# Kernel tuning notes

Hardware: AMD Instinct MI355X
Metric: run time of the kernel (lower is better)

The kernel has to match this reference:

```python
import jax, jax.numpy as jnp
import numpy as np

NUM_EXPERTS = 8
TOP_K = 2
RMS_EPS = 1e-6
SCALING = NUM_EXPERTS / TOP_K


def setup_inputs() -> dict:
    key = jax.random.key(0)
    ks = jax.random.split(key, 6)
    B, S, H, I, E = 4, 2048, 2048, 1024, NUM_EXPERTS
    return {
        "hidden_states": jax.random.normal(ks[0], (B, S, H), dtype=jnp.float32),
        "norm_w": jnp.ones((H,), dtype=jnp.float32),
        "router_w": jax.random.normal(ks[1], (E, H), dtype=jnp.float32) * 0.02,
        "gate_w": jax.random.normal(ks[2], (E, I, H), dtype=jnp.float32) * 0.02,
        "up_w": jax.random.normal(ks[3], (E, I, H), dtype=jnp.float32) * 0.02,
        "down_w": jax.random.normal(ks[4], (E, H, I), dtype=jnp.float32) * 0.02,
    }


def reference(hidden_states, norm_w, router_w, gate_w, up_w, down_w):
    B, S, H = hidden_states.shape
    T = B * S
    flat = hidden_states.reshape(T, H)

    # RMSNorm on router input (fp32 math, as in torch module)
    x32 = flat.astype(jnp.float32)
    var = jnp.mean(x32 * x32, axis=-1, keepdims=True)
    router_input = norm_w * (x32 * jax.lax.rsqrt(var + RMS_EPS))

    # Router: softmax -> top-k -> renormalize
    logits = router_input @ router_w.T                     # [T, E]
    probs = jax.nn.softmax(logits, axis=-1)
    topw, topi = jax.lax.top_k(probs, TOP_K)               # [T, K]
    topw = topw / jnp.sum(topw, axis=-1, keepdims=True)

    # Expert combine: per-token weight for expert e (0 if not selected).
    # Running every token through every expert with weight-0 masking is
    # mathematically identical to the gather/scatter dispatch.
    out = jnp.zeros_like(flat)
    for e in range(NUM_EXPERTS):
        w_e = jnp.sum(jnp.where(topi == e, topw, 0.0), axis=-1)   # [T]
        g = flat @ gate_w[e].T                                    # [T, I]
        u = flat @ up_w[e].T                                      # [T, I]
        o = (jax.nn.silu(g) * u) @ down_w[e].T                    # [T, H]
        out = out + o * w_e[:, None]

    student_output = out.reshape(B, S, H) * SCALING

    # Aux load-balancing loss (training path)
    importance = jnp.sum(probs, axis=0) / T                       # [E]
    load = jnp.sum(topi[..., None] == jnp.arange(NUM_EXPERTS), axis=(0, 1)) / (T * TOP_K)
    aux_loss = jnp.sum(importance * load.astype(jnp.float32)) * NUM_EXPERTS

    return student_output, aux_loss
```

## Files before the change

### kernel.cpp

```cpp
#include <hip/hip_runtime.h>
#include <hip/hip_bf16.h>
#include <cstdint>

#define T_TOKENS 8192
#define H_DIM 2048
#define I_DIM 1024
#define N_EXPERTS 8
#define PAIRS (T_TOKENS * 2)
#define TOT_TILES 144
#define TOT_ROWS (TOT_TILES * 128)

using f32x4 = __attribute__((ext_vector_type(4))) float;
using bfv   = __attribute__((ext_vector_type(8))) short;
using u16x8 = __attribute__((ext_vector_type(8))) unsigned short;

typedef __attribute__((address_space(3))) unsigned int lds_u32;
typedef __attribute__((address_space(1))) unsigned int glb_u32;

__device__ __forceinline__ void gll16(const void* g, void* l) {
  __builtin_amdgcn_global_load_lds((const glb_u32*)g, (lds_u32*)l, 16, 0, 0);
}
#define SB0() __builtin_amdgcn_sched_barrier(0)
#define BAR() __builtin_amdgcn_s_barrier()

__device__ inline unsigned short f2bf(float f) {
  unsigned int u = __float_as_uint(f);
  u += 0x7FFFu + ((u >> 16) & 1u);
  return (unsigned short)(u >> 16);
}
__device__ inline float bf2f(unsigned short u) {
  return __uint_as_float((unsigned int)u << 16);
}

__global__ __launch_bounds__(256) void moe_convert_kernel(
    const float* __restrict__ src, unsigned short* __restrict__ dst, int n8) {
  int i = blockIdx.x * 256 + threadIdx.x;
  if (i >= n8) return;
  size_t o = (size_t)i * 8;
  f32x4 a = *reinterpret_cast<const f32x4*>(src + o);
  f32x4 b = *reinterpret_cast<const f32x4*>(src + o + 4);
  u16x8 r = {f2bf(a[0]), f2bf(a[1]), f2bf(a[2]), f2bf(a[3]),
             f2bf(b[0]), f2bf(b[1]), f2bf(b[2]), f2bf(b[3])};
  *reinterpret_cast<u16x8*>(dst + o) = r;
}

__global__ __launch_bounds__(256) void moe_router_kernel(
    const float* __restrict__ X, const float* __restrict__ norm_w,
    const float* __restrict__ rw, float* __restrict__ probs,
    float* __restrict__ topw, int* __restrict__ topi,
    unsigned int* __restrict__ counts, unsigned short* __restrict__ Xb,
    const float* __restrict__ gate_w, const float* __restrict__ up_w,
    const float* __restrict__ down_w,
    unsigned short* __restrict__ W1, unsigned short* __restrict__ W2,
    unsigned short* __restrict__ W3) {
  int t = blockIdx.x;
  int tid = threadIdx.x;
  {
    size_t co = (size_t)t * 2048 + tid * 8;
    f32x4 a = *reinterpret_cast<const f32x4*>(gate_w + co);
    f32x4 b = *reinterpret_cast<const f32x4*>(gate_w + co + 4);
    u16x8 r = {f2bf(a[0]), f2bf(a[1]), f2bf(a[2]), f2bf(a[3]),
               f2bf(b[0]), f2bf(b[1]), f2bf(b[2]), f2bf(b[3])};
    *reinterpret_cast<u16x8*>(W1 + co) = r;
    a = *reinterpret_cast<const f32x4*>(up_w + co);
    b = *reinterpret_cast<const f32x4*>(up_w + co + 4);
    u16x8 r2 = {f2bf(a[0]), f2bf(a[1]), f2bf(a[2]), f2bf(a[3]),
                f2bf(b[0]), f2bf(b[1]), f2bf(b[2]), f2bf(b[3])};
    *reinterpret_cast<u16x8*>(W2 + co) = r2;
    if (W3) {
      a = *reinterpret_cast<const f32x4*>(down_w + co);
      b = *reinterpret_cast<const f32x4*>(down_w + co + 4);
      u16x8 r3 = {f2bf(a[0]), f2bf(a[1]), f2bf(a[2]), f2bf(a[3]),
                  f2bf(b[0]), f2bf(b[1]), f2bf(b[2]), f2bf(b[3])};
      *reinterpret_cast<u16x8*>(W3 + co) = r3;
    }
  }
  const float* x = X + (size_t)t * H_DIM;
  int base = tid * 8;
  f32x4 v0 = *reinterpret_cast<const f32x4*>(x + base);
  f32x4 v1 = *reinterpret_cast<const f32x4*>(x + base + 4);
  u16x8 bx = {f2bf(v0[0]), f2bf(v0[1]), f2bf(v0[2]), f2bf(v0[3]),
              f2bf(v1[0]), f2bf(v1[1]), f2bf(v1[2]), f2bf(v1[3])};
  *reinterpret_cast<u16x8*>(Xb + (size_t)t * H_DIM + base) = bx;
  f32x4 nw0 = *reinterpret_cast<const f32x4*>(norm_w + base);
  f32x4 nw1 = *reinterpret_cast<const f32x4*>(norm_w + base + 4);
  float vals[9];
  vals[0] = v0[0]*v0[0] + v0[1]*v0[1] + v0[2]*v0[2] + v0[3]*v0[3]
          + v1[0]*v1[0] + v1[1]*v1[1] + v1[2]*v1[2] + v1[3]*v1[3];
  f32x4 a0 = v0 * nw0, a1 = v1 * nw1;
#pragma unroll
  for (int e = 0; e < 8; ++e) {
    const float* r = rw + e * H_DIM + base;
    f32x4 r0 = *reinterpret_cast<const f32x4*>(r);
    f32x4 r1 = *reinterpret_cast<const f32x4*>(r + 4);
    f32x4 d = a0 * r0 + a1 * r1;
    vals[e + 1] = d[0] + d[1] + d[2] + d[3];
  }
#pragma unroll
  for (int v = 0; v < 9; ++v) {
    float s = vals[v];
#pragma unroll
    for (int off = 32; off > 0; off >>= 1) s += __shfl_xor(s, off);
    vals[v] = s;
  }
  __shared__ float red[4][9];
  int lane = tid & 63, w = tid >> 6;
  if (lane == 0) {
#pragma unroll
    for (int v = 0; v < 9; ++v) red[w][v] = vals[v];
  }
  __syncthreads();
  if (tid == 0) {
    float tot[9];
#pragma unroll
    for (int v = 0; v < 9; ++v) tot[v] = red[0][v] + red[1][v] + red[2][v] + red[3][v];
    float rs = rsqrtf(tot[0] / (float)H_DIM + 1e-6f);
    float lg[8], mx = -1e30f;
#pragma unroll
    for (int e = 0; e < 8; ++e) { lg[e] = tot[e + 1] * rs; mx = fmaxf(mx, lg[e]); }
    float pe[8], sum = 0.f;
#pragma unroll
    for (int e = 0; e < 8; ++e) { pe[e] = expf(lg[e] - mx); sum += pe[e]; }
    float inv = 1.f / sum;
#pragma unroll
    for (int e = 0; e < 8; ++e) { pe[e] *= inv; probs[t * 8 + e] = pe[e]; }
    int b1 = 0; float p1 = pe[0];
#pragma unroll
    for (int e = 1; e < 8; ++e) if (pe[e] > p1) { p1 = pe[e]; b1 = e; }
    int b2 = -1; float p2 = -1.f;
#pragma unroll
    for (int e = 0; e < 8; ++e) if (e != b1 && pe[e] > p2) { p2 = pe[e]; b2 = e; }
    float wsum = p1 + p2;
    topw[t * 2] = p1 / wsum;
    topw[t * 2 + 1] = p2 / wsum;
    topi[t * 2] = b1;
    topi[t * 2 + 1] = b2;
    atomicAdd(&counts[b1], 1u);
    atomicAdd(&counts[8 + b2], 1u);
  }
}

__global__ __launch_bounds__(256) void moe_importance_kernel(
    const float* __restrict__ probs, float* __restrict__ impSum) {
  int e = blockIdx.x, tid = threadIdx.x;
  float s = 0.f;
  for (int t = tid; t < T_TOKENS; t += 256) s += probs[t * 8 + e];
  __shared__ float red[256];
  red[tid] = s;
  __syncthreads();
  for (int st = 128; st > 0; st >>= 1) {
    if (tid < st) red[tid] += red[tid + st];
    __syncthreads();
  }
  if (tid == 0) impSum[e] = red[0];
}

__global__ void moe_offsets_aux_kernel(const unsigned int* __restrict__ counts,
                                       const float* __restrict__ impSum,
                                       int* __restrict__ tileOff,
                                       float* __restrict__ out_aux) {
  if (threadIdx.x == 0 && blockIdx.x == 0) {
    int acc = 0;
    for (int b = 0; b < 16; ++b) {
      tileOff[b] = acc;
      acc += (int)((counts[b] + 127u) >> 7);
    }
    tileOff[16] = acc;
    float a = 0.f;
    for (int e = 0; e < 8; ++e) {
      float load = (float)(counts[e] + counts[8 + e]) / (float)PAIRS;
      a += (impSum[e] / (float)T_TOKENS) * load;
    }
    out_aux[0] = a * (float)N_EXPERTS;
  }
}

__global__ __launch_bounds__(256) void moe_assign_kernel(
    const int* __restrict__ topi, const int* __restrict__ tileOff,
    unsigned int* __restrict__ cursors, int* __restrict__ row2pair) {
  int p = blockIdx.x * 256 + threadIdx.x;
  if (p >= PAIRS) return;
  int b = topi[p] + 8 * (p & 1);
  unsigned int pos = atomicAdd(&cursors[b], 1u);
  row2pair[tileOff[b] * 128 + (int)pos] = p;
}


__global__ __launch_bounds__(256, 4) void moe_stage_a(
    const unsigned short* __restrict__ Xb,
    const unsigned short* __restrict__ Wg, const unsigned short* __restrict__ Wu,
    const int* __restrict__ row2pair, const int* __restrict__ tileOff,
    unsigned int* __restrict__ workCtr, unsigned short* __restrict__ P) {
  __shared__ __align__(16) unsigned short sAB[16384];
  __shared__ int sTok[128];
  __shared__ int sWork;
  const int tid = threadIdx.x;
  const int lane = tid & 63, w = tid >> 6;
  const int wm = w >> 1, wn = w & 1;
  const int lrow = lane & 15, grp = lane >> 4;
  const int sub = lane >> 3;
  const int kcs = ((lane & 7) ^ sub) << 3;
  const int cx = (lane & 7) << 3;
  const int nTiles = tileOff[16];
  const int nWork = nTiles * 16;

  for (;;) {
    if (tid == 0) sWork = (int)atomicAdd(workCtr, 1u);
    __syncthreads();
    const int item = sWork;
    if (item >= nWork) break;
    const int mt = item >> 4;
    const int nt = item & 15;
    int b = 0;
#pragma unroll
    for (int k = 1; k < 16; ++k) if (tileOff[k] <= mt) b = k;
    const int e = b & 7;
    const int row0 = mt * 128;
    if (tid < 128) {
      int pr = row2pair[row0 + tid];
      sTok[tid] = (pr >= 0) ? (pr >> 1) : 0;
    }
    __syncthreads();

    const size_t wbase = (size_t)e * ((size_t)I_DIM * H_DIM);
    const unsigned short* src[8];
#pragma unroll
    for (int i = 0; i < 4; ++i) {
      int row = i * 32 + 8 * w + sub;
      src[i] = Xb + (size_t)sTok[row] * H_DIM + kcs;
    }
#pragma unroll
    for (int i = 4; i < 8; ++i) {
      int brow = (i - 4) * 32 + 8 * w + sub;
      int wq = brow >> 6, r6 = brow & 63;
      int ic = nt * 64 + wq * 32 + (r6 & 31);
      const unsigned short* bp = (r6 & 32) ? Wu : Wg;
      src[i] = bp + wbase + (size_t)ic * H_DIM + kcs;
    }

    f32x4 acc[4][4] = {};

#pragma unroll 1
    for (int kk = 0; kk < 32; ++kk) {
#pragma unroll
      for (int i = 0; i < 8; ++i)
        gll16(src[i] + (kk << 6), (void*)&sAB[(i * 256 + tid) * 8]);
      SB0();
      asm volatile("s_waitcnt vmcnt(0)" ::: "memory");
      SB0();
      BAR();
      SB0();
#pragma unroll
      for (int ks = 0; ks < 2; ++ks) {
        const int co = ((ks * 4 + grp) << 3) ^ cx;
        bfv af[4], bf[4];
#pragma unroll
        for (int m = 0; m < 4; ++m)
          af[m] = *reinterpret_cast<const bfv*>(
              &sAB[(wm * 64 + m * 16 + lrow) * 64 + co]);
#pragma unroll
        for (int n = 0; n < 4; ++n)
          bf[n] = *reinterpret_cast<const bfv*>(
              &sAB[8192 + (wn * 64 + n * 16 + lrow) * 64 + co]);
        __builtin_amdgcn_s_setprio(1);
#pragma unroll
        for (int m = 0; m < 4; ++m)
#pragma unroll
          for (int n = 0; n < 4; ++n)
            acc[m][n] = __builtin_amdgcn_mfma_f32_16x16x32_bf16(af[m], bf[n], acc[m][n], 0, 0, 0);
        __builtin_amdgcn_s_setprio(0);
      }
      SB0();
      BAR();
    }

#pragma unroll
    for (int m = 0; m < 4; ++m) {
#pragma unroll
      for (int n = 0; n < 2; ++n) {
#pragma unroll
        for (int j = 0; j < 4; ++j) {
          float g = acc[m][n][j];
          float uu = acc[m][n + 2][j];
          float pv = (g / (1.f + expf(-g))) * uu;
          int row = row0 + wm * 64 + m * 16 + grp * 4 + j;
          int col = nt * 64 + wn * 32 + n * 16 + lrow;
          P[(size_t)row * I_DIM + col] = f2bf(pv);
        }
      }
    }
  }
}

__global__ __launch_bounds__(256, 4) void moe_stage_b(
    const unsigned short* __restrict__ Pb, const unsigned short* __restrict__ Wd,
    const int* __restrict__ row2pair, const int* __restrict__ tileOff,
    unsigned int* __restrict__ workCtr, unsigned short* __restrict__ Opairs) {
  __shared__ __align__(16) unsigned short sAB[16384];
  __shared__ int sPair[128];
  __shared__ int sWork;
  const int tid = threadIdx.x;
  const int lane = tid & 63, w = tid >> 6;
  const int wm = w >> 1, wn = w & 1;
  const int lrow = lane & 15, grp = lane >> 4;
  const int sub = lane >> 3;
  const int kcs = ((lane & 7) ^ sub) << 3;
  const int cx = (lane & 7) << 3;
  const int nTiles = tileOff[16];
  const int nWork = nTiles * 16;

  for (;;) {
    if (tid == 0) sWork = (int)atomicAdd(workCtr, 1u);
    __syncthreads();
    const int item = sWork;
    if (item >= nWork) break;
    const int mt = item >> 4;
    const int nt = item & 15;
    int b = 0;
#pragma unroll
    for (int k = 1; k < 16; ++k) if (tileOff[k] <= mt) b = k;
    const int e = b & 7;
    const int row0 = mt * 128, h0 = nt * 128;
    if (tid < 128) sPair[tid] = row2pair[row0 + tid];
    __syncthreads();

    const unsigned short* src[8];
#pragma unroll
    for (int i = 0; i < 4; ++i) {
      int row = i * 32 + 8 * w + sub;
      src[i] = Pb + (size_t)(row0 + row) * I_DIM + kcs;
    }
#pragma unroll
    for (int i = 4; i < 8; ++i) {
      int brow = (i - 4) * 32 + 8 * w + sub;
      src[i] = Wd + (size_t)e * ((size_t)H_DIM * I_DIM) + (size_t)(h0 + brow) * I_DIM + kcs;
    }

    f32x4 acc[4][4] = {};

#pragma unroll 1
    for (int kk = 0; kk < 16; ++kk) {
#pragma unroll
      for (int i = 0; i < 8; ++i)
        gll16(src[i] + (kk << 6), (void*)&sAB[(i * 256 + tid) * 8]);
      SB0();
      asm volatile("s_waitcnt vmcnt(0)" ::: "memory");
      SB0();
      BAR();
      SB0();
#pragma unroll
      for (int ks = 0; ks < 2; ++ks) {
        const int co = ((ks * 4 + grp) << 3) ^ cx;
        bfv af[4], bf[4];
#pragma unroll
        for (int m = 0; m < 4; ++m)
          af[m] = *reinterpret_cast<const bfv*>(
              &sAB[(wm * 64 + m * 16 + lrow) * 64 + co]);
#pragma unroll
        for (int n = 0; n < 4; ++n)
          bf[n] = *reinterpret_cast<const bfv*>(
              &sAB[8192 + (wn * 64 + n * 16 + lrow) * 64 + co]);
        __builtin_amdgcn_s_setprio(1);
#pragma unroll
        for (int m = 0; m < 4; ++m)
#pragma unroll
          for (int n = 0; n < 4; ++n)
            acc[m][n] = __builtin_amdgcn_mfma_f32_16x16x32_bf16(af[m], bf[n], acc[m][n], 0, 0, 0);
        __builtin_amdgcn_s_setprio(0);
      }
      SB0();
      BAR();
    }

#pragma unroll
    for (int m = 0; m < 4; ++m) {
#pragma unroll
      for (int j = 0; j < 4; ++j) {
        int rl = wm * 64 + m * 16 + grp * 4 + j;
        int pr = sPair[rl];
        if (pr < 0) continue;
        unsigned short* orow = Opairs + (size_t)pr * H_DIM + h0 + wn * 64 + lrow;
#pragma unroll
        for (int n = 0; n < 4; ++n) orow[n * 16] = f2bf(acc[m][n][j]);
      }
    }
  }
}

__global__ __launch_bounds__(256) void moe_combine_kernel(
    const unsigned short* __restrict__ Opairs, const float* __restrict__ topw,
    float* __restrict__ out) {
  size_t g = (size_t)blockIdx.x * 256 + threadIdx.x;
  size_t base = g * 8;
  int t = (int)(base >> 11);
  int h = (int)(base & 2047);
  float w0 = topw[t * 2] * 4.f;
  float w1 = topw[t * 2 + 1] * 4.f;
  u16x8 o0 = *reinterpret_cast<const u16x8*>(Opairs + (size_t)(t * 2) * H_DIM + h);
  u16x8 o1 = *reinterpret_cast<const u16x8*>(Opairs + (size_t)(t * 2 + 1) * H_DIM + h);
  f32x4 r0, r1;
#pragma unroll
  for (int j = 0; j < 4; ++j) r0[j] = w0 * bf2f(o0[j]) + w1 * bf2f(o1[j]);
#pragma unroll
  for (int j = 0; j < 4; ++j) r1[j] = w0 * bf2f(o0[4 + j]) + w1 * bf2f(o1[4 + j]);
  *reinterpret_cast<f32x4*>(out + base) = r0;
  *reinterpret_cast<f32x4*>(out + base + 4) = r1;
}

extern "C" void kernel_launch(void* const* d_in, const int* in_sizes, int n_in,
                              void* d_out, int out_size, void* d_ws, size_t ws_size,
                              hipStream_t stream) {
  const float* X = (const float*)d_in[0];
  const float* norm_w = (const float*)d_in[1];
  const float* router_w = (const float*)d_in[2];
  const float* gate_w = (const float*)d_in[3];
  const float* up_w = (const float*)d_in[4];
  const float* down_w = (const float*)d_in[5];
  float* out = (float*)d_out;

  char* ws = (char*)d_ws;
  unsigned short* P = (unsigned short*)(ws);
  float* probs = (float*)(ws + 37748736);
  float* topw = (float*)(ws + 38010880);
  int* topi = (int*)(ws + 38076416);
  int* row2pair = (int*)(ws + 38141952);
  char* ctrl = ws + 38215680;
  unsigned int* counts = (unsigned int*)(ctrl);
  unsigned int* cursors = (unsigned int*)(ctrl + 64);
  float* impSum = (float*)(ctrl + 128);
  int* tileOff = (int*)(ctrl + 192);
  unsigned int* wcA = (unsigned int*)(ctrl + 384);
  unsigned int* wcB = (unsigned int*)(ctrl + 388);
  unsigned short* W1 = (unsigned short*)(ws + 38216192);
  unsigned short* W2 = (unsigned short*)(ws + 71770624);
  unsigned short* Xb = (unsigned short*)(ws + 105325056);
  unsigned short* Opairs = (unsigned short*)(ws + 71770624);
  unsigned short* W3 = (unsigned short*)(ws + 138879488);
  const bool w3ok = ws_size >= 172433920ull;

  hipMemsetAsync(ctrl, 0, 512, stream);
  hipMemsetAsync(row2pair, 0xFF, (size_t)TOT_ROWS * 4, stream);

  moe_router_kernel<<<T_TOKENS, 256, 0, stream>>>(
      X, norm_w, router_w, probs, topw, topi, counts, Xb,
      gate_w, up_w, down_w, W1, W2, w3ok ? W3 : nullptr);
  moe_importance_kernel<<<N_EXPERTS, 256, 0, stream>>>(probs, impSum);
  moe_offsets_aux_kernel<<<1, 64, 0, stream>>>(counts, impSum, tileOff, out + 16777216);
  moe_assign_kernel<<<PAIRS / 256, 256, 0, stream>>>(topi, tileOff, cursors, row2pair);

  moe_stage_a<<<1024, 256, 0, stream>>>(Xb, W1, W2, row2pair, tileOff, wcA, P);

  const unsigned short* DW = W3;
  if (!w3ok) {
    const int N8 = (N_EXPERTS * I_DIM * H_DIM) / 8;
    moe_convert_kernel<<<N8 / 256, 256, 0, stream>>>(down_w, W1, N8);
    DW = W1;
  }
  moe_stage_b<<<1024, 256, 0, stream>>>(P, DW, row2pair, tileOff, wcB, Opairs);
  moe_combine_kernel<<<T_TOKENS, 256, 0, stream>>>(Opairs, topw, out);
}
```

Baseline: 623.2 us.

## Use 512-thread 128x256 tiles with 3-stage LDS prefetch pipeline in expert GEMMs

Both expert GEMM stages now run 512-thread workgroups that each compute a 128x256 output tile, doubling the N extent per work item and halving the number of items. Global-to-LDS loads are triple-buffered: three K-slices are issued up front and each iteration waits only for the oldest one (partial vmcnt) before prefetching the slice three steps ahead. This targets the exposed memory latency of the old load-then-wait-all loop and cuts redundant A-tile reloads. In exchange it uses much more LDS per block with one block per CU, and fewer, larger work items may balance less evenly across CUs.

```diff
diff --git a/kernel.cpp b/kernel.cpp
--- a/kernel.cpp
+++ b/kernel.cpp
@@ -9,6 +9,7 @@
 #define PAIRS (T_TOKENS * 2)
 #define TOT_TILES 144
 #define TOT_ROWS (TOT_TILES * 128)
+#define SLOT 24576
 
 using f32x4 = __attribute__((ext_vector_type(4))) float;
 using bfv   = __attribute__((ext_vector_type(8))) short;
@@ -186,31 +187,30 @@
 }
 
 
-__global__ __launch_bounds__(256, 4) void moe_stage_a(
+__global__ __launch_bounds__(512, 1) void moe_stage_a(
     const unsigned short* __restrict__ Xb,
     const unsigned short* __restrict__ Wg, const unsigned short* __restrict__ Wu,
     const int* __restrict__ row2pair, const int* __restrict__ tileOff,
     unsigned int* __restrict__ workCtr, unsigned short* __restrict__ P) {
-  __shared__ __align__(16) unsigned short sAB[16384];
+  __shared__ __align__(16) unsigned short sAB[3 * SLOT];
   __shared__ int sTok[128];
   __shared__ int sWork;
   const int tid = threadIdx.x;
   const int lane = tid & 63, w = tid >> 6;
-  const int wm = w >> 1, wn = w & 1;
+  const int wm = w >> 2, wn = w & 3;
   const int lrow = lane & 15, grp = lane >> 4;
-  const int sub = lane >> 3;
-  const int kcs = ((lane & 7) ^ sub) << 3;
+  const int r8 = tid >> 3, j8 = tid & 7;
   const int cx = (lane & 7) << 3;
   const int nTiles = tileOff[16];
-  const int nWork = nTiles * 16;
+  const int nWork = nTiles * 8;
 
   for (;;) {
     if (tid == 0) sWork = (int)atomicAdd(workCtr, 1u);
     __syncthreads();
     const int item = sWork;
     if (item >= nWork) break;
-    const int mt = item >> 4;
-    const int nt = item & 15;
+    const int mt = item >> 3;
+    const int nt = item & 7;
     int b = 0;
 #pragma unroll
     for (int k = 1; k < 16; ++k) if (tileOff[k] <= mt) b = k;
@@ -223,30 +223,41 @@
     __syncthreads();
 
     const size_t wbase = (size_t)e * ((size_t)I_DIM * H_DIM);
-    const unsigned short* src[8];
-#pragma unroll
-    for (int i = 0; i < 4; ++i) {
-      int row = i * 32 + 8 * w + sub;
-      src[i] = Xb + (size_t)sTok[row] * H_DIM + kcs;
-    }
-#pragma unroll
-    for (int i = 4; i < 8; ++i) {
-      int brow = (i - 4) * 32 + 8 * w + sub;
-      int wq = brow >> 6, r6 = brow & 63;
-      int ic = nt * 64 + wq * 32 + (r6 & 31);
-      const unsigned short* bp = (r6 & 32) ? Wu : Wg;
-      src[i] = bp + wbase + (size_t)ic * H_DIM + kcs;
+    const unsigned short* sA[2];
+    const unsigned short* sB[4];
+#pragma unroll
+    for (int i = 0; i < 2; ++i) {
+      int row = i * 64 + r8;
+      sA[i] = Xb + (size_t)sTok[row] * H_DIM + ((j8 ^ (row & 7)) << 3);
+    }
+    {
+      const unsigned short* bp = (r8 & 32) ? Wu : Wg;
+#pragma unroll
+      for (int i = 0; i < 4; ++i) {
+        int ic = nt * 128 + i * 32 + (r8 & 31);
+        sB[i] = bp + wbase + (size_t)ic * H_DIM + ((j8 ^ (r8 & 7)) << 3);
+      }
     }
 
     f32x4 acc[4][4] = {};
 
+#pragma unroll
+    for (int t = 0; t < 3; ++t) {
+      const int so = t * SLOT;
+#pragma unroll
+      for (int i = 0; i < 2; ++i)
+        gll16(sA[i] + (t << 6), (void*)&sAB[so + (i * 512 + tid) * 8]);
+#pragma unroll
+      for (int i = 0; i < 4; ++i)
+        gll16(sB[i] + (t << 6), (void*)&sAB[so + 8192 + (i * 512 + tid) * 8]);
+    }
+
+    int so = 0;
 #pragma unroll 1
     for (int kk = 0; kk < 32; ++kk) {
-#pragma unroll
-      for (int i = 0; i < 8; ++i)
-        gll16(src[i] + (kk << 6), (void*)&sAB[(i * 256 + tid) * 8]);
-      SB0();
-      asm volatile("s_waitcnt vmcnt(0)" ::: "memory");
+      if (kk < 30)      { asm volatile("s_waitcnt vmcnt(12)" ::: "memory"); }
+      else if (kk == 30){ asm volatile("s_waitcnt vmcnt(6)" ::: "memory"); }
+      else              { asm volatile("s_waitcnt vmcnt(0)" ::: "memory"); }
       SB0();
       BAR();
       SB0();
@@ -257,11 +268,11 @@
 #pragma unroll
         for (int m = 0; m < 4; ++m)
           af[m] = *reinterpret_cast<const bfv*>(
-              &sAB[(wm * 64 + m * 16 + lrow) * 64 + co]);
+              &sAB[so + (wm * 64 + m * 16 + lrow) * 64 + co]);
 #pragma unroll
         for (int n = 0; n < 4; ++n)
           bf[n] = *reinterpret_cast<const bfv*>(
-              &sAB[8192 + (wn * 64 + n * 16 + lrow) * 64 + co]);
+              &sAB[so + 8192 + (wn * 64 + n * 16 + lrow) * 64 + co]);
         __builtin_amdgcn_s_setprio(1);
 #pragma unroll
         for (int m = 0; m < 4; ++m)
@@ -272,6 +283,18 @@
       }
       SB0();
       BAR();
+      SB0();
+      if (kk + 3 < 32) {
+        const int t = kk + 3;
+#pragma unroll
+        for (int i = 0; i < 2; ++i)
+          gll16(sA[i] + (t << 6), (void*)&sAB[so + (i * 512 + tid) * 8]);
+#pragma unroll
+        for (int i = 0; i < 4; ++i)
+          gll16(sB[i] + (t << 6), (void*)&sAB[so + 8192 + (i * 512 + tid) * 8]);
+      }
+      so += SLOT;
+      if (so == 3 * SLOT) so = 0;
     }
 
 #pragma unroll
@@ -284,7 +307,7 @@
           float uu = acc[m][n + 2][j];
           float pv = (g / (1.f + expf(-g))) * uu;
           int row = row0 + wm * 64 + m * 16 + grp * 4 + j;
-          int col = nt * 64 + wn * 32 + n * 16 + lrow;
+          int col = nt * 128 + wn * 32 + n * 16 + lrow;
           P[(size_t)row * I_DIM + col] = f2bf(pv);
         }
       }
@@ -292,59 +315,70 @@
   }
 }
 
-__global__ __launch_bounds__(256, 4) void moe_stage_b(
+__global__ __launch_bounds__(512, 1) void moe_stage_b(
     const unsigned short* __restrict__ Pb, const unsigned short* __restrict__ Wd,
     const int* __restrict__ row2pair, const int* __restrict__ tileOff,
     unsigned int* __restrict__ workCtr, unsigned short* __restrict__ Opairs) {
-  __shared__ __align__(16) unsigned short sAB[16384];
+  __shared__ __align__(16) unsigned short sAB[3 * SLOT];
   __shared__ int sPair[128];
   __shared__ int sWork;
   const int tid = threadIdx.x;
   const int lane = tid & 63, w = tid >> 6;
-  const int wm = w >> 1, wn = w & 1;
+  const int wm = w >> 2, wn = w & 3;
   const int lrow = lane & 15, grp = lane >> 4;
-  const int sub = lane >> 3;
-  const int kcs = ((lane & 7) ^ sub) << 3;
+  const int r8 = tid >> 3, j8 = tid & 7;
   const int cx = (lane & 7) << 3;
   const int nTiles = tileOff[16];
-  const int nWork = nTiles * 16;
+  const int nWork = nTiles * 8;
 
   for (;;) {
     if (tid == 0) sWork = (int)atomicAdd(workCtr, 1u);
     __syncthreads();
     const int item = sWork;
     if (item >= nWork) break;
-    const int mt = item >> 4;
-    const int nt = item & 15;
+    const int mt = item >> 3;
+    const int nt = item & 7;
     int b = 0;
 #pragma unroll
     for (int k = 1; k < 16; ++k) if (tileOff[k] <= mt) b = k;
     const int e = b & 7;
-    const int row0 = mt * 128, h0 = nt * 128;
+    const int row0 = mt * 128, h0 = nt * 256;
     if (tid < 128) sPair[tid] = row2pair[row0 + tid];
     __syncthreads();
 
-    const unsigned short* src[8];
+    const unsigned short* sA[2];
+    const unsigned short* sB[4];
+#pragma unroll
+    for (int i = 0; i < 2; ++i) {
+      int row = i * 64 + r8;
+      sA[i] = Pb + (size_t)(row0 + row) * I_DIM + ((j8 ^ (row & 7)) << 3);
+    }
 #pragma unroll
     for (int i = 0; i < 4; ++i) {
-      int row = i * 32 + 8 * w + sub;
-      src[i] = Pb + (size_t)(row0 + row) * I_DIM + kcs;
-    }
-#pragma unroll
-    for (int i = 4; i < 8; ++i) {
-      int brow = (i - 4) * 32 + 8 * w + sub;
-      src[i] = Wd + (size_t)e * ((size_t)H_DIM * I_DIM) + (size_t)(h0 + brow) * I_DIM + kcs;
+      int brow = i * 64 + r8;
+      sB[i] = Wd + (size_t)e * ((size_t)H_DIM * I_DIM) +
+              (size_t)(h0 + brow) * I_DIM + ((j8 ^ (r8 & 7)) << 3);
     }
 
     f32x4 acc[4][4] = {};
 
+#pragma unroll
+    for (int t = 0; t < 3; ++t) {
+      const int so = t * SLOT;
+#pragma unroll
+      for (int i = 0; i < 2; ++i)
+        gll16(sA[i] + (t << 6), (void*)&sAB[so + (i * 512 + tid) * 8]);
+#pragma unroll
+      for (int i = 0; i < 4; ++i)
+        gll16(sB[i] + (t << 6), (void*)&sAB[so + 8192 + (i * 512 + tid) * 8]);
+    }
+
+    int so = 0;
 #pragma unroll 1
     for (int kk = 0; kk < 16; ++kk) {
-#pragma unroll
-      for (int i = 0; i < 8; ++i)
-        gll16(src[i] + (kk << 6), (void*)&sAB[(i * 256 + tid) * 8]);
-      SB0();
-      asm volatile("s_waitcnt vmcnt(0)" ::: "memory");
+      if (kk < 14)      { asm volatile("s_waitcnt vmcnt(12)" ::: "memory"); }
+      else if (kk == 14){ asm volatile("s_waitcnt vmcnt(6)" ::: "memory"); }
+      else              { asm volatile("s_waitcnt vmcnt(0)" ::: "memory"); }
       SB0();
       BAR();
       SB0();
@@ -355,11 +389,11 @@
 #pragma unroll
         for (int m = 0; m < 4; ++m)
           af[m] = *reinterpret_cast<const bfv*>(
-              &sAB[(wm * 64 + m * 16 + lrow) * 64 + co]);
+              &sAB[so + (wm * 64 + m * 16 + lrow) * 64 + co]);
 #pragma unroll
         for (int n = 0; n < 4; ++n)
           bf[n] = *reinterpret_cast<const bfv*>(
-              &sAB[8192 + (wn * 64 + n * 16 + lrow) * 64 + co]);
+              &sAB[so + 8192 + (wn * 64 + n * 16 + lrow) * 64 + co]);
         __builtin_amdgcn_s_setprio(1);
 #pragma unroll
         for (int m = 0; m < 4; ++m)
@@ -370,6 +404,18 @@
       }
       SB0();
       BAR();
+      SB0();
+      if (kk + 3 < 16) {
+        const int t = kk + 3;
+#pragma unroll
+        for (int i = 0; i < 2; ++i)
+          gll16(sA[i] + (t << 6), (void*)&sAB[so + (i * 512 + tid) * 8]);
+#pragma unroll
+        for (int i = 0; i < 4; ++i)
+          gll16(sB[i] + (t << 6), (void*)&sAB[so + 8192 + (i * 512 + tid) * 8]);
+      }
+      so += SLOT;
+      if (so == 3 * SLOT) so = 0;
     }
 
 #pragma unroll
@@ -448,7 +494,7 @@
   moe_offsets_aux_kernel<<<1, 64, 0, stream>>>(counts, impSum, tileOff, out + 16777216);
   moe_assign_kernel<<<PAIRS / 256, 256, 0, stream>>>(topi, tileOff, cursors, row2pair);
 
-  moe_stage_a<<<1024, 256, 0, stream>>>(Xb, W1, W2, row2pair, tileOff, wcA, P);
+  moe_stage_a<<<256, 512, 0, stream>>>(Xb, W1, W2, row2pair, tileOff, wcA, P);
 
   const unsigned short* DW = W3;
   if (!w3ok) {
@@ -456,6 +502,6 @@
     moe_convert_kernel<<<N8 / 256, 256, 0, stream>>>(down_w, W1, N8);
     DW = W1;
   }
-  moe_stage_b<<<1024, 256, 0, stream>>>(P, DW, row2pair, tileOff, wcB, Opairs);
+  moe_stage_b<<<256, 512, 0, stream>>>(P, DW, row2pair, tileOff, wcB, Opairs);
   moe_combine_kernel<<<T_TOKENS, 256, 0, stream>>>(Opairs, topw, out);
 }
```

New measurement: 634.0 us. No clear change (+1.7%).

## Replace atomic work queue with XCD-aware static tile mapping; widen stage B tile

Applied to the files above, without the earlier changes.

Both grouped GEMM stages drop the persistent atomic work-counter loop and launch one block per (m-tile, n-tile). The block index is remapped so that consecutive m-tiles, and the n-tiles sharing them, land on the same XCD, which should improve L2 reuse of activations and expert weights. Stage B also widens its N tile from 128 to 256 columns, using 12 loads per k-step, 48KB of LDS and a 4x8 accumulator per warp at 3 blocks/CU, so the P rows are re-read fewer times. In exchange, blocks beyond the real tile count exit immediately, there is no longer dynamic load balancing, and stage B carries more register pressure with lower occupancy.

```diff
diff --git a/kernel.cpp b/kernel.cpp
--- a/kernel.cpp
+++ b/kernel.cpp
@@ -190,10 +190,9 @@
     const unsigned short* __restrict__ Xb,
     const unsigned short* __restrict__ Wg, const unsigned short* __restrict__ Wu,
     const int* __restrict__ row2pair, const int* __restrict__ tileOff,
-    unsigned int* __restrict__ workCtr, unsigned short* __restrict__ P) {
+    unsigned short* __restrict__ P) {
   __shared__ __align__(16) unsigned short sAB[16384];
   __shared__ int sTok[128];
-  __shared__ int sWork;
   const int tid = threadIdx.x;
   const int lane = tid & 63, w = tid >> 6;
   const int wm = w >> 1, wn = w & 1;
@@ -202,103 +201,100 @@
   const int kcs = ((lane & 7) ^ sub) << 3;
   const int cx = (lane & 7) << 3;
   const int nTiles = tileOff[16];
-  const int nWork = nTiles * 16;
-
-  for (;;) {
-    if (tid == 0) sWork = (int)atomicAdd(workCtr, 1u);
-    __syncthreads();
-    const int item = sWork;
-    if (item >= nWork) break;
-    const int mt = item >> 4;
-    const int nt = item & 15;
-    int b = 0;
-#pragma unroll
-    for (int k = 1; k < 16; ++k) if (tileOff[k] <= mt) b = k;
-    const int e = b & 7;
-    const int row0 = mt * 128;
-    if (tid < 128) {
-      int pr = row2pair[row0 + tid];
-      sTok[tid] = (pr >= 0) ? (pr >> 1) : 0;
-    }
-    __syncthreads();
-
-    const size_t wbase = (size_t)e * ((size_t)I_DIM * H_DIM);
-    const unsigned short* src[8];
-#pragma unroll
-    for (int i = 0; i < 4; ++i) {
-      int row = i * 32 + 8 * w + sub;
-      src[i] = Xb + (size_t)sTok[row] * H_DIM + kcs;
-    }
-#pragma unroll
-    for (int i = 4; i < 8; ++i) {
-      int brow = (i - 4) * 32 + 8 * w + sub;
-      int wq = brow >> 6, r6 = brow & 63;
-      int ic = nt * 64 + wq * 32 + (r6 & 31);
-      const unsigned short* bp = (r6 & 32) ? Wu : Wg;
-      src[i] = bp + wbase + (size_t)ic * H_DIM + kcs;
-    }
-
-    f32x4 acc[4][4] = {};
+
+  const int b = blockIdx.x;
+  const int xcd = b & 7, j = b >> 3;
+  const int grpl = j / 48, r = j % 48;
+  const int mtl = r >> 4, nt = r & 15;
+  const int mt = (xcd * 6 + grpl) * 3 + mtl;
+  if (mt >= nTiles) return;
+
+  int bb = 0;
+#pragma unroll
+  for (int k = 1; k < 16; ++k) if (tileOff[k] <= mt) bb = k;
+  const int e = bb & 7;
+  const int row0 = mt * 128;
+  if (tid < 128) {
+    int pr = row2pair[row0 + tid];
+    sTok[tid] = (pr >= 0) ? (pr >> 1) : 0;
+  }
+  __syncthreads();
+
+  const size_t wbase = (size_t)e * ((size_t)I_DIM * H_DIM);
+  const unsigned short* src[8];
+#pragma unroll
+  for (int i = 0; i < 4; ++i) {
+    int row = i * 32 + 8 * w + sub;
+    src[i] = Xb + (size_t)sTok[row] * H_DIM + kcs;
+  }
+#pragma unroll
+  for (int i = 4; i < 8; ++i) {
+    int brow = (i - 4) * 32 + 8 * w + sub;
+    int wq = brow >> 6, r6 = brow & 63;
+    int ic = nt * 64 + wq * 32 + (r6 & 31);
+    const unsigned short* bp = (r6 & 32) ? Wu : Wg;
+    src[i] = bp + wbase + (size_t)ic * H_DIM + kcs;
+  }
+
+  f32x4 acc[4][4] = {};
 
 #pragma unroll 1
-    for (int kk = 0; kk < 32; ++kk) {
-#pragma unroll
-      for (int i = 0; i < 8; ++i)
-        gll16(src[i] + (kk << 6), (void*)&sAB[(i * 256 + tid) * 8]);
-      SB0();
-      asm volatile("s_waitcnt vmcnt(0)" ::: "memory");
-      SB0();
-      BAR();
-      SB0();
-#pragma unroll
-      for (int ks = 0; ks < 2; ++ks) {
-        const int co = ((ks * 4 + grp) << 3) ^ cx;
-        bfv af[4], bf[4];
-#pragma unroll
-        for (int m = 0; m < 4; ++m)
-          af[m] = *reinterpret_cast<const bfv*>(
-              &sAB[(wm * 64 + m * 16 + lrow) * 64 + co]);
+  for (int kk = 0; kk < 32; ++kk) {
+#pragma unroll
+    for (int i = 0; i < 8; ++i)
+      gll16(src[i] + (kk << 6), (void*)&sAB[(i * 256 + tid) * 8]);
+    SB0();
+    asm volatile("s_waitcnt vmcnt(0)" ::: "memory");
+    SB0();
+    BAR();
+    SB0();
+#pragma unroll
+    for (int ks = 0; ks < 2; ++ks) {
+      const int co = ((ks * 4 + grp) << 3) ^ cx;
+      bfv af[4], bf[4];
+#pragma unroll
+      for (int m = 0; m < 4; ++m)
+        af[m] = *reinterpret_cast<const bfv*>(
+            &sAB[(wm * 64 + m * 16 + lrow) * 64 + co]);
+#pragma unroll
+      for (int n = 0; n < 4; ++n)
+        bf[n] = *reinterpret_cast<const bfv*>(
+            &sAB[8192 + (wn * 64 + n * 16 + lrow) * 64 + co]);
+      __builtin_amdgcn_s_setprio(1);
+#pragma unroll
+      for (int m = 0; m < 4; ++m)
 #pragma unroll
         for (int n = 0; n < 4; ++n)
-          bf[n] = *reinterpret_cast<const bfv*>(
-              &sAB[8192 + (wn * 64 + n * 16 + lrow) * 64 + co]);
-        __builtin_amdgcn_s_setprio(1);
-#pragma unroll
-        for (int m = 0; m < 4; ++m)
-#pragma unroll
-          for (int n = 0; n < 4; ++n)
-            acc[m][n] = __builtin_amdgcn_mfma_f32_16x16x32_bf16(af[m], bf[n], acc[m][n], 0, 0, 0);
-        __builtin_amdgcn_s_setprio(0);
+          acc[m][n] = __builtin_amdgcn_mfma_f32_16x16x32_bf16(af[m], bf[n], acc[m][n], 0, 0, 0);
+      __builtin_amdgcn_s_setprio(0);
+    }
+    SB0();
+    BAR();
+  }
+
+#pragma unroll
+  for (int m = 0; m < 4; ++m) {
+#pragma unroll
+    for (int n = 0; n < 2; ++n) {
+#pragma unroll
+      for (int jj = 0; jj < 4; ++jj) {
+        float g = acc[m][n][jj];
+        float uu = acc[m][n + 2][jj];
+        float pv = (g / (1.f + expf(-g))) * uu;
+        int row = row0 + wm * 64 + m * 16 + grp * 4 + jj;
+        int col = nt * 64 + wn * 32 + n * 16 + lrow;
+        P[(size_t)row * I_DIM + col] = f2bf(pv);
       }
-      SB0();
-      BAR();
-    }
-
-#pragma unroll
-    for (int m = 0; m < 4; ++m) {
-#pragma unroll
-      for (int n = 0; n < 2; ++n) {
-#pragma unroll
-        for (int j = 0; j < 4; ++j) {
-          float g = acc[m][n][j];
-          float uu = acc[m][n + 2][j];
-          float pv = (g / (1.f + expf(-g))) * uu;
-          int row = row0 + wm * 64 + m * 16 + grp * 4 + j;
-          int col = nt * 64 + wn * 32 + n * 16 + lrow;
-          P[(size_t)row * I_DIM + col] = f2bf(pv);
-        }
-      }
-    }
-  }
-}
-
-__global__ __launch_bounds__(256, 4) void moe_stage_b(
+    }
+  }
+}
+
+__global__ __launch_bounds__(256, 3) void moe_stage_b(
     const unsigned short* __restrict__ Pb, const unsigned short* __restrict__ Wd,
     const int* __restrict__ row2pair, const int* __restrict__ tileOff,
-    unsigned int* __restrict__ workCtr, unsigned short* __restrict__ Opairs) {
-  __shared__ __align__(16) unsigned short sAB[16384];
+    unsigned short* __restrict__ Opairs) {
+  __shared__ __align__(16) unsigned short sAB[24576];
   __shared__ int sPair[128];
-  __shared__ int sWork;
   const int tid = threadIdx.x;
   const int lane = tid & 63, w = tid >> 6;
   const int wm = w >> 1, wn = w & 1;
@@ -307,82 +303,80 @@
   const int kcs = ((lane & 7) ^ sub) << 3;
   const int cx = (lane & 7) << 3;
   const int nTiles = tileOff[16];
-  const int nWork = nTiles * 16;
-
-  for (;;) {
-    if (tid == 0) sWork = (int)atomicAdd(workCtr, 1u);
-    __syncthreads();
-    const int item = sWork;
-    if (item >= nWork) break;
-    const int mt = item >> 4;
-    const int nt = item & 15;
-    int b = 0;
-#pragma unroll
-    for (int k = 1; k < 16; ++k) if (tileOff[k] <= mt) b = k;
-    const int e = b & 7;
-    const int row0 = mt * 128, h0 = nt * 128;
-    if (tid < 128) sPair[tid] = row2pair[row0 + tid];
-    __syncthreads();
-
-    const unsigned short* src[8];
-#pragma unroll
-    for (int i = 0; i < 4; ++i) {
-      int row = i * 32 + 8 * w + sub;
-      src[i] = Pb + (size_t)(row0 + row) * I_DIM + kcs;
-    }
-#pragma unroll
-    for (int i = 4; i < 8; ++i) {
-      int brow = (i - 4) * 32 + 8 * w + sub;
-      src[i] = Wd + (size_t)e * ((size_t)H_DIM * I_DIM) + (size_t)(h0 + brow) * I_DIM + kcs;
-    }
-
-    f32x4 acc[4][4] = {};
+
+  const int b = blockIdx.x;
+  const int xcd = b & 7, j = b >> 3;
+  const int grpl = j / 24, r = j % 24;
+  const int mtl = r >> 3, nt = r & 7;
+  const int mt = (xcd * 6 + grpl) * 3 + mtl;
+  if (mt >= nTiles) return;
+
+  int bb = 0;
+#pragma unroll
+  for (int k = 1; k < 16; ++k) if (tileOff[k] <= mt) bb = k;
+  const int e = bb & 7;
+  const int row0 = mt * 128, h0 = nt * 256;
+  if (tid < 128) sPair[tid] = row2pair[row0 + tid];
+  __syncthreads();
+
+  const unsigned short* src[12];
+#pragma unroll
+  for (int i = 0; i < 4; ++i) {
+    int row = i * 32 + 8 * w + sub;
+    src[i] = Pb + (size_t)(row0 + row) * I_DIM + kcs;
+  }
+#pragma unroll
+  for (int i = 4; i < 12; ++i) {
+    int brow = (i - 4) * 32 + 8 * w + sub;
+    src[i] = Wd + (size_t)e * ((size_t)H_DIM * I_DIM) + (size_t)(h0 + brow) * I_DIM + kcs;
+  }
+
+  f32x4 acc[4][8] = {};
 
 #pragma unroll 1
-    for (int kk = 0; kk < 16; ++kk) {
-#pragma unroll
-      for (int i = 0; i < 8; ++i)
-        gll16(src[i] + (kk << 6), (void*)&sAB[(i * 256 + tid) * 8]);
-      SB0();
-      asm volatile("s_waitcnt vmcnt(0)" ::: "memory");
-      SB0();
-      BAR();
-      SB0();
-#pragma unroll
-      for (int ks = 0; ks < 2; ++ks) {
-        const int co = ((ks * 4 + grp) << 3) ^ cx;
-        bfv af[4], bf[4];
-#pragma unroll
-        for (int m = 0; m < 4; ++m)
-          af[m] = *reinterpret_cast<const bfv*>(
-              &sAB[(wm * 64 + m * 16 + lrow) * 64 + co]);
-#pragma unroll
-        for (int n = 0; n < 4; ++n)
-          bf[n] = *reinterpret_cast<const bfv*>(
-              &sAB[8192 + (wn * 64 + n * 16 + lrow) * 64 + co]);
-        __builtin_amdgcn_s_setprio(1);
-#pragma unroll
-        for (int m = 0; m < 4; ++m)
-#pragma unroll
-          for (int n = 0; n < 4; ++n)
-            acc[m][n] = __builtin_amdgcn_mfma_f32_16x16x32_bf16(af[m], bf[n], acc[m][n], 0, 0, 0);
-        __builtin_amdgcn_s_setprio(0);
-      }
-      SB0();
-      BAR();
-    }
-
-#pragma unroll
-    for (int m = 0; m < 4; ++m) {
-#pragma unroll
-      for (int j = 0; j < 4; ++j) {
-        int rl = wm * 64 + m * 16 + grp * 4 + j;
-        int pr = sPair[rl];
-        if (pr < 0) continue;
-        unsigned short* orow = Opairs + (size_t)pr * H_DIM + h0 + wn * 64 + lrow;
-#pragma unroll
-        for (int n = 0; n < 4; ++n) orow[n * 16] = f2bf(acc[m][n][j]);
-      }
+  for (int kk = 0; kk < 16; ++kk) {
+#pragma unroll
+    for (int i = 0; i < 12; ++i)
+      gll16(src[i] + (kk << 6), (void*)&sAB[(i * 256 + tid) * 8]);
+    SB0();
+    asm volatile("s_waitcnt vmcnt(0)" ::: "memory");
+    SB0();
+    BAR();
+    SB0();
+#pragma unroll
+    for (int ks = 0; ks < 2; ++ks) {
+      const int co = ((ks * 4 + grp) << 3) ^ cx;
+      bfv af[4], bf[8];
+#pragma unroll
+      for (int m = 0; m < 4; ++m)
+        af[m] = *reinterpret_cast<const bfv*>(
+            &sAB[(wm * 64 + m * 16 + lrow) * 64 + co]);
+#pragma unroll
+      for (int n = 0; n < 8; ++n)
+        bf[n] = *reinterpret_cast<const bfv*>(
+            &sAB[8192 + (wn * 128 + n * 16 + lrow) * 64 + co]);
+      __builtin_amdgcn_s_setprio(1);
+#pragma unroll
+      for (int m = 0; m < 4; ++m)
+#pragma unroll
+        for (int n = 0; n < 8; ++n)
+          acc[m][n] = __builtin_amdgcn_mfma_f32_16x16x32_bf16(af[m], bf[n], acc[m][n], 0, 0, 0);
+      __builtin_amdgcn_s_setprio(0);
+    }
+    SB0();
+    BAR();
+  }
+
+#pragma unroll
+  for (int m = 0; m < 4; ++m) {
+#pragma unroll
+    for (int jj = 0; jj < 4; ++jj) {
+      int rl = wm * 64 + m * 16 + grp * 4 + jj;
+      int pr = sPair[rl];
+      if (pr < 0) continue;
+      unsigned short* orow = Opairs + (size_t)pr * H_DIM + h0 + wn * 128 + lrow;
+#pragma unroll
+      for (int n = 0; n < 8; ++n) orow[n * 16] = f2bf(acc[m][n][jj]);
     }
   }
 }
@@ -429,8 +423,6 @@
   unsigned int* cursors = (unsigned int*)(ctrl + 64);
   float* impSum = (float*)(ctrl + 128);
   int* tileOff = (int*)(ctrl + 192);
-  unsigned int* wcA = (unsigned int*)(ctrl + 384);
-  unsigned int* wcB = (unsigned int*)(ctrl + 388);
   unsigned short* W1 = (unsigned short*)(ws + 38216192);
   unsigned short* W2 = (unsigned short*)(ws + 71770624);
   unsigned short* Xb = (unsigned short*)(ws + 105325056);
@@ -448,7 +440,7 @@
   moe_offsets_aux_kernel<<<1, 64, 0, stream>>>(counts, impSum, tileOff, out + 16777216);
   moe_assign_kernel<<<PAIRS / 256, 256, 0, stream>>>(topi, tileOff, cursors, row2pair);
 
-  moe_stage_a<<<1024, 256, 0, stream>>>(Xb, W1, W2, row2pair, tileOff, wcA, P);
+  moe_stage_a<<<TOT_TILES * 16, 256, 0, stream>>>(Xb, W1, W2, row2pair, tileOff, P);
 
   const unsigned short* DW = W3;
   if (!w3ok) {
@@ -456,6 +448,6 @@
     moe_convert_kernel<<<N8 / 256, 256, 0, stream>>>(down_w, W1, N8);
     DW = W1;
   }
-  moe_stage_b<<<1024, 256, 0, stream>>>(P, DW, row2pair, tileOff, wcB, Opairs);
+  moe_stage_b<<<TOT_TILES * 8, 256, 0, stream>>>(P, DW, row2pair, tileOff, Opairs);
   moe_combine_kernel<<<T_TOKENS, 256, 0, stream>>>(Opairs, topw, out);
 }
```

Measured after the change: 966.3 us. 1.55x slower.
